# Kernel tuning notes

Measured on AMD Instinct MI355X. Metric: run time of the kernel, lower is better.

Reference implementation:

```python
import jax, jax.numpy as jnp
import numpy as np

N_G, N_U, E, C = 100000, 100000, 3200000, 2000000


def graph_conv(x, edges, W_rel, W_root, b):
    # PyG GraphConv (aggr='add'): out_i = (sum_{j->i} x_j) @ W_rel + x_i @ W_root + b
    src, dst = edges[0], edges[1]
    agg = jax.ops.segment_sum(x[src], dst, num_segments=x.shape[0])
    return agg @ W_rel + x @ W_root + b


def setup_inputs() -> dict:
    key = jax.random.key(0)
    ks = jax.random.split(key, 16)
    d = {
        'x_u': jax.random.normal(ks[0], (N_U, 4), jnp.float32),
        'x_g': jax.random.normal(ks[1], (N_G, 4), jnp.float32),
        'candidates': jax.random.randint(ks[2], (C, 2), 0, N_G + N_U, jnp.int64),
        'edges': jax.random.randint(ks[3], (2, E), 0, N_G, jnp.int64),
        # GraphConv(4,8)
        'W1_rel': jax.random.normal(ks[4], (4, 8), jnp.float32) * 0.5,
        'W1_root': jax.random.normal(ks[5], (4, 8), jnp.float32) * 0.5,
        'b1': jax.random.normal(ks[6], (8,), jnp.float32) * 0.1,
        # GraphConv(8,16)
        'W2_rel': jax.random.normal(ks[7], (8, 16), jnp.float32) * 0.35,
        'W2_root': jax.random.normal(ks[8], (8, 16), jnp.float32) * 0.35,
        'b2': jax.random.normal(ks[9], (16,), jnp.float32) * 0.1,
        # fc_unconnected: Linear(4,16) (Dropout is identity in eval)
        'W_un': jax.random.normal(ks[10], (4, 16), jnp.float32) * 0.5,
        'b_un': jax.random.normal(ks[11], (16,), jnp.float32) * 0.1,
        # fc: Linear(32,64) -> SELU -> Linear(64,1)
        'W_fc1': jax.random.normal(ks[12], (32, 64), jnp.float32) * 0.18,
        'b_fc1': jax.random.normal(ks[13], (64,), jnp.float32) * 0.1,
        'W_fc2': jax.random.normal(ks[14], (64, 1), jnp.float32) * 0.12,
        'b_fc2': jax.random.normal(ks[15], (1,), jnp.float32) * 0.1,
    }
    return d


def reference(x_u, x_g, candidates, edges,
              W1_rel, W1_root, b1, W2_rel, W2_root, b2,
              W_un, b_un, W_fc1, b_fc1, W_fc2, b_fc2):
    x_unconnected = x_u @ W_un + b_un                      # [N_u, 16]
    h = jax.nn.selu(graph_conv(x_g, edges, W1_rel, W1_root, b1))   # [N_g, 8]
    x_graph = jax.nn.selu(graph_conv(h, edges, W2_rel, W2_root, b2))  # [N_g, 16]
    x_stacked = jnp.concatenate([x_graph, x_unconnected], axis=0)  # [N_g+N_u, 16]
    ec = jnp.concatenate([x_stacked[candidates[:, 0]],
                          x_stacked[candidates[:, 1]]], axis=1)    # [C, 32]
    hidden = jax.nn.selu(ec @ W_fc1 + b_fc1)               # [C, 64]
    out = (hidden @ W_fc2 + b_fc2).squeeze(-1)             # [C]
    return out


if __name__ == '__main__':
    print(reference(**setup_inputs()).shape)
```

## Files before the change

### kernel.cpp

```cpp
#include <hip/hip_runtime.h>
#include <hip/hip_bf16.h>

#define NG 100000
#define NU 100000
#define NE 3200000
#define NC 2000000

#define BSZ 128
#define NBK 782
#define CAP 5120

#define NSUP 61
#define SFB 13
#define SSPAN (SFB * BSZ)
#define SCAP 56320
#define B1CH 4096
#define B2CH 4096

typedef __attribute__((ext_vector_type(8))) short short8;
typedef __attribute__((ext_vector_type(4))) float floatx4;
typedef unsigned short ushortx8 __attribute__((ext_vector_type(8)));

__device__ __forceinline__ float selu_f(float x) {
    const float LAM = 1.0507009873554805f;
    const float ALA = 1.7580993408473766f;
    const float L2E = 1.44269504088896340736f;
    float e = __builtin_amdgcn_exp2f(fminf(x, 0.f) * L2E);
    return fmaf(LAM, fmaxf(x, 0.f), fmaf(ALA, e, -ALA));
}

__device__ __forceinline__ float bfbits2f(unsigned short u) {
    return __uint_as_float(((unsigned)u) << 16);
}

__device__ __forceinline__ unsigned short f2bfbits(float f) {
    union { __hip_bfloat16 h; unsigned short u; } cv;
    cv.h = __float2bfloat16(f);
    return cv.u;
}

__device__ __forceinline__ float ldf(const void* p, int i, int isbf) {
    return isbf ? bfbits2f(((const unsigned short*)p)[i]) : ((const float*)p)[i];
}

__global__ void k_detect(const unsigned int* __restrict__ xw,
                         const unsigned int* __restrict__ cw,
                         const unsigned int* __restrict__ ew,
                         int* __restrict__ flags) {
    if (threadIdx.x != 0 || blockIdx.x != 0) return;
    int nb = 0;
    for (int i = 0; i < 64; ++i) {
        unsigned lo = xw[i] & 0xffffu;
        unsigned e = (lo >> 7) & 0xff;
        if (e >= 112 && e <= 134) ++nb;
    }
    flags[0] = (nb >= 32) ? 1 : 0;
    int cz = 0, ez = 0;
    for (int i = 0; i < 64; ++i) {
        if (cw[2 * i + 1] == 0u) ++cz;
        if (ew[2 * i + 1] == 0u) ++ez;
    }
    flags[1] = (cz >= 48) ? 1 : 0;
    flags[2] = (ez >= 48) ? 1 : 0;
}

__device__ __forceinline__ void ld_edge(const void* edges, long long e, int e64,
                                        int& s, int& d) {
    if (e64) {
        const long long* el = (const long long*)edges;
        s = (int)el[e];
        d = (int)el[NE + e];
    } else {
        const int* ei = (const int*)edges;
        s = ei[e];
        d = ei[NE + e];
    }
}

__global__ __launch_bounds__(256) void k_bin1(const void* __restrict__ edges,
        int* __restrict__ scur, unsigned int* __restrict__ slist,
        const int* __restrict__ flags) {
    __shared__ unsigned int tmp[B1CH];
    __shared__ unsigned char tsup[B1CH];
    __shared__ unsigned int ord[B1CH];
    __shared__ unsigned char osup[B1CH];
    __shared__ int hist[64];
    __shared__ int lstart[64];
    __shared__ int ofs[64];
    __shared__ int gbase[64];

    int tid = threadIdx.x;
    long long base = (long long)blockIdx.x * B1CH;
    int chunk = (int)(NE - base);
    if (chunk > B1CH) chunk = B1CH;
    int e64 = flags[2];

    if (tid < 64) hist[tid] = 0;
    __syncthreads();

    for (int i = 0; i < B1CH / 256; ++i) {
        int idx = i * 256 + tid;
        if (idx < chunk) {
            int s, d;
            ld_edge(edges, base + idx, e64, s, d);
            int sup = d / SSPAN;
            tmp[idx] = ((unsigned)s << 11) | (unsigned)(d - sup * SSPAN);
            tsup[idx] = (unsigned char)sup;
            atomicAdd(&hist[sup], 1);
        }
    }
    __syncthreads();

    if (tid == 0) {
        int run = 0;
        for (int b = 0; b < NSUP; ++b) {
            lstart[b] = run;
            run += hist[b];
        }
    }
    __syncthreads();
    if (tid < NSUP) {
        int c = hist[tid];
        int g = 0;
        if (c > 0) g = atomicAdd(&scur[tid], c);
        gbase[tid] = g;
        ofs[tid] = lstart[tid];
    }
    __syncthreads();

    for (int i = 0; i < B1CH / 256; ++i) {
        int idx = i * 256 + tid;
        if (idx < chunk) {
            int sup = tsup[idx];
            int pos = atomicAdd(&ofs[sup], 1);
            ord[pos] = tmp[idx];
            osup[pos] = (unsigned char)sup;
        }
    }
    __syncthreads();

    for (int i = 0; i < B1CH / 256; ++i) {
        int idx = i * 256 + tid;
        if (idx < chunk) {
            int sup = osup[idx];
            int p = gbase[sup] + (idx - lstart[sup]);
            if (p < SCAP) slist[(long long)sup * SCAP + p] = ord[idx];
        }
    }
}

#define SCH2 ((SCAP + B2CH - 1) / B2CH)

__global__ __launch_bounds__(256) void k_bin2(const int* __restrict__ scur,
        const unsigned int* __restrict__ slist,
        int* __restrict__ gcur, unsigned int* __restrict__ glist) {
    __shared__ unsigned int tmp[B2CH];
    __shared__ unsigned int ord[B2CH];
    __shared__ unsigned char ofid[B2CH];
    __shared__ int hist[16];
    __shared__ int lstart[16];
    __shared__ int ofs[16];
    __shared__ int gbase[16];

    int tid = threadIdx.x;
    int sup = blockIdx.x / SCH2;
    int ch = blockIdx.x % SCH2;
    int scnt = scur[sup];
    if (scnt > SCAP) scnt = SCAP;
    int start = ch * B2CH;
    int cnt = scnt - start;
    if (cnt <= 0) return;
    if (cnt > B2CH) cnt = B2CH;
    const unsigned int* sp = slist + (long long)sup * SCAP + start;

    if (tid < 16) hist[tid] = 0;
    __syncthreads();

    for (int i = 0; i < B2CH / 256; ++i) {
        int idx = i * 256 + tid;
        if (idx < cnt) {
            unsigned u = sp[idx];
            tmp[idx] = u;
            atomicAdd(&hist[(u & 2047) >> 7], 1);
        }
    }
    __syncthreads();

    if (tid == 0) {
        int run = 0;
        for (int b = 0; b < SFB; ++b) {
            lstart[b] = run;
            run += hist[b];
        }
    }
    __syncthreads();
    if (tid < SFB) {
        int c = hist[tid];
        int g = 0;
        int bf = sup * SFB + tid;
        if (c > 0 && bf < NBK) g = atomicAdd(&gcur[bf], c);
        gbase[tid] = g;
        ofs[tid] = lstart[tid];
    }
    __syncthreads();

    for (int i = 0; i < B2CH / 256; ++i) {
        int idx = i * 256 + tid;
        if (idx < cnt) {
            unsigned u = tmp[idx];
            int dl = u & 2047;
            int f = dl >> 7;
            int pos = atomicAdd(&ofs[f], 1);
            ord[pos] = ((u >> 11) << 7) | (unsigned)(dl & 127);
            ofid[pos] = (unsigned char)f;
        }
    }
    __syncthreads();

    for (int i = 0; i < B2CH / 256; ++i) {
        int idx = i * 256 + tid;
        if (idx < cnt) {
            int f = ofid[idx];
            int bf = sup * SFB + f;
            int p = gbase[f] + (idx - lstart[f]);
            if (p < CAP) glist[(long long)bf * CAP + p] = ord[idx];
        }
    }
}

__global__ __launch_bounds__(256) void k_sort(const int* __restrict__ gcur,
        unsigned int* __restrict__ glist,
        int* __restrict__ dstoff, int* __restrict__ ddeg) {
    __shared__ unsigned int tmp[CAP];
    __shared__ unsigned int sorted[CAP];
    __shared__ int hist[BSZ];
    __shared__ int incl[BSZ];
    __shared__ int cur[BSZ];
    int b = blockIdx.x;
    int tid = threadIdx.x;
    int cnt = gcur[b];
    if (cnt > CAP) cnt = CAP;
    unsigned int* lp = glist + (long long)b * CAP;

    if (tid < BSZ) hist[tid] = 0;
    __syncthreads();
    for (int k = tid; k < cnt; k += 256) {
        unsigned u = lp[k];
        tmp[k] = u;
        atomicAdd(&hist[u & 127], 1);
    }
    __syncthreads();
    if (tid < BSZ) incl[tid] = hist[tid];
    __syncthreads();
    for (int off = 1; off < BSZ; off <<= 1) {
        int v = (tid < BSZ && tid >= off) ? incl[tid - off] : 0;
        __syncthreads();
        if (tid < BSZ && tid >= off) incl[tid] += v;
        __syncthreads();
    }
    if (tid < BSZ) {
        int excl = incl[tid] - hist[tid];
        cur[tid] = excl;
        int d = b * BSZ + tid;
        if (d < NG) {
            dstoff[d] = b * CAP + excl;
            ddeg[d] = hist[tid];
        }
    }
    __syncthreads();
    for (int k = tid; k < cnt; k += 256) {
        unsigned u = tmp[k];
        int pos = atomicAdd(&cur[u & 127], 1);
        sorted[pos] = u >> 7;
    }
    __syncthreads();
    for (int k = tid; k < cnt; k += 256) lp[k] = sorted[k];
}

__global__ __launch_bounds__(256) void k_gather1(const int* __restrict__ dstoff,
        const int* __restrict__ ddeg, const unsigned int* __restrict__ glist,
        const void* __restrict__ xg,
        const void* __restrict__ W1r, const void* __restrict__ W1o,
        const void* __restrict__ b1, unsigned short* __restrict__ hbf,
        const int* __restrict__ flags) {
    int gid = blockIdx.x * 256 + threadIdx.x;
    int d = gid >> 4;
    if (d >= NG) return;
    int q = gid & 15;
    int isbf = flags[0];
    int start = dstoff[d];
    int deg = ddeg[d];
    float a0 = 0.f, a1 = 0.f, a2 = 0.f, a3 = 0.f;
    if (isbf) {
        const unsigned short* xp = (const unsigned short*)xg;
        int k = q;
        for (; k + 16 < deg; k += 32) {
            int s0 = glist[start + k];
            int s1 = glist[start + k + 16];
            ushort4 r0 = *(const ushort4*)(xp + s0 * 4);
            ushort4 r1 = *(const ushort4*)(xp + s1 * 4);
            a0 += bfbits2f(r0.x) + bfbits2f(r1.x);
            a1 += bfbits2f(r0.y) + bfbits2f(r1.y);
            a2 += bfbits2f(r0.z) + bfbits2f(r1.z);
            a3 += bfbits2f(r0.w) + bfbits2f(r1.w);
        }
        for (; k < deg; k += 16) {
            int s = glist[start + k];
            ushort4 r = *(const ushort4*)(xp + s * 4);
            a0 += bfbits2f(r.x); a1 += bfbits2f(r.y);
            a2 += bfbits2f(r.z); a3 += bfbits2f(r.w);
        }
    } else {
        const float* xp = (const float*)xg;
        int k = q;
        for (; k + 16 < deg; k += 32) {
            int s0 = glist[start + k];
            int s1 = glist[start + k + 16];
            float4 r0 = *(const float4*)(xp + s0 * 4);
            float4 r1 = *(const float4*)(xp + s1 * 4);
            a0 += r0.x + r1.x;
            a1 += r0.y + r1.y;
            a2 += r0.z + r1.z;
            a3 += r0.w + r1.w;
        }
        for (; k < deg; k += 16) {
            int s = glist[start + k];
            float4 r = *(const float4*)(xp + s * 4);
            a0 += r.x; a1 += r.y; a2 += r.z; a3 += r.w;
        }
    }
#pragma unroll
    for (int off = 1; off < 16; off <<= 1) {
        a0 += __shfl_xor(a0, off);
        a1 += __shfl_xor(a1, off);
        a2 += __shfl_xor(a2, off);
        a3 += __shfl_xor(a3, off);
    }
    if (q < 8) {
        float a[4] = {a0, a1, a2, a3};
        float v = ldf(b1, q, isbf);
#pragma unroll
        for (int c = 0; c < 4; ++c)
            v += a[c] * ldf(W1r, c * 8 + q, isbf)
               + ldf(xg, d * 4 + c, isbf) * ldf(W1o, c * 8 + q, isbf);
        hbf[d * 8 + q] = f2bfbits(selu_f(v));
    }
}

__global__ __launch_bounds__(256) void k_gather2(const int* __restrict__ dstoff,
        const int* __restrict__ ddeg, const unsigned int* __restrict__ glist,
        const ushortx8* __restrict__ hbf,
        const void* __restrict__ W2r, const void* __restrict__ W2o,
        const void* __restrict__ b2, unsigned short* __restrict__ xs,
        const int* __restrict__ flags) {
    int gid = blockIdx.x * 256 + threadIdx.x;
    int d = gid >> 4;
    if (d >= NG) return;
    int q = gid & 15;
    int isbf = flags[0];
    int start = dstoff[d];
    int deg = ddeg[d];
    float a[8] = {0.f, 0.f, 0.f, 0.f, 0.f, 0.f, 0.f, 0.f};
    int k = q;
    for (; k + 16 < deg; k += 32) {
        int s0 = glist[start + k];
        int s1 = glist[start + k + 16];
        ushortx8 r0 = hbf[s0];
        ushortx8 r1 = hbf[s1];
#pragma unroll
        for (int c = 0; c < 8; ++c)
            a[c] += bfbits2f((unsigned short)r0[c]) + bfbits2f((unsigned short)r1[c]);
    }
    for (; k < deg; k += 16) {
        int s = glist[start + k];
        ushortx8 r = hbf[s];
#pragma unroll
        for (int c = 0; c < 8; ++c) a[c] += bfbits2f((unsigned short)r[c]);
    }
#pragma unroll
    for (int off = 1; off < 16; off <<= 1) {
#pragma unroll
        for (int c = 0; c < 8; ++c) a[c] += __shfl_xor(a[c], off);
    }
    ushortx8 hr = hbf[d];
    float hv[8];
#pragma unroll
    for (int c = 0; c < 8; ++c) hv[c] = bfbits2f((unsigned short)hr[c]);
    float v = ldf(b2, q, isbf);
#pragma unroll
    for (int c = 0; c < 8; ++c)
        v += a[c] * ldf(W2r, c * 16 + q, isbf)
           + hv[c] * ldf(W2o, c * 16 + q, isbf);
    xs[d * 16 + q] = f2bfbits(selu_f(v));
}

__global__ __launch_bounds__(256) void k_unconn(const void* __restrict__ xu,
        const void* __restrict__ Wun, const void* __restrict__ bun,
        unsigned short* __restrict__ xs, const int* __restrict__ flags) {
    int u = blockIdx.x * 256 + threadIdx.x;
    if (u >= NU) return;
    int isbf = flags[0];
    float x[4];
#pragma unroll
    for (int k = 0; k < 4; ++k) x[k] = ldf(xu, u * 4 + k, isbf);
    ushortx8 lo, hi;
#pragma unroll
    for (int j = 0; j < 16; ++j) {
        float v = ldf(bun, j, isbf);
#pragma unroll
        for (int k = 0; k < 4; ++k)
            v += x[k] * ldf(Wun, k * 16 + j, isbf);
        unsigned short bb = f2bfbits(v);
        if (j < 8) lo[j] = bb; else hi[j - 8] = bb;
    }
    ushortx8* xp = (ushortx8*)(xs + (NG + u) * 16);
    xp[0] = lo;
    xp[1] = hi;
}

__device__ __forceinline__ int ld_candrow(const void* cand, int c, int hp, int c64) {
    const int* ci = (const int*)cand;
    return c64 ? ci[(2 * c + hp) * 2] : ci[2 * c + hp];
}

__global__ __launch_bounds__(256, 5) void k_fc(const unsigned short* __restrict__ xs,
        const void* __restrict__ cand,
        const void* __restrict__ Wfc1, const void* __restrict__ bfc1,
        const void* __restrict__ Wfc2, const void* __restrict__ bfc2,
        void* __restrict__ out, const int* __restrict__ flags) {
    const float LAM = 1.0507009873554805f;
    const float ALA = 1.7580993408473766f;
    const float L2E = 1.44269504088896340736f;
    const float AR2 = 1.6732632423543772f * 1.44269504088896340736f;
    const float SCL = 1.0507009873554805f / 1.44269504088896340736f;
    int lane = threadIdx.x & 63;
    int wid = (blockIdx.x * blockDim.x + threadIdx.x) >> 6;
    int m = lane & 15;
    int half = lane >> 4;
    int isbf = flags[0], c64 = flags[1];

    short8 wfrag[4];
    floatx4 cbias[4];
    float w2s[4][4];
    float c_corr;
    if (isbf) {
        const unsigned short* W1p = (const unsigned short*)Wfc1;
#pragma unroll
        for (int t = 0; t < 4; ++t)
#pragma unroll
            for (int j = 0; j < 8; ++j)
                wfrag[t][j] = (short)f2bfbits(
                    bfbits2f(W1p[(half * 8 + j) * 64 + t * 16 + m]) * L2E);
        const unsigned short* b1p = (const unsigned short*)bfc1;
        const unsigned short* w2p = (const unsigned short*)Wfc2;
        float asum = 0.f;
#pragma unroll
        for (int t = 0; t < 4; ++t)
#pragma unroll
            for (int r = 0; r < 4; ++r) {
                int h = t * 16 + half * 4 + r;
                cbias[t][r] = bfbits2f(b1p[h]) * L2E;
                float w2 = bfbits2f(w2p[h]);
                w2s[t][r] = w2 * SCL;
                asum += w2 * ALA;
            }
        asum += __shfl_xor(asum, 16, 64);
        asum += __shfl_xor(asum, 32, 64);
        c_corr = bfbits2f(((const unsigned short*)bfc2)[0]) - asum;
    } else {
        const float* W1p = (const float*)Wfc1;
#pragma unroll
        for (int t = 0; t < 4; ++t)
#pragma unroll
            for (int j = 0; j < 8; ++j)
                wfrag[t][j] = (short)f2bfbits(
                    W1p[(half * 8 + j) * 64 + t * 16 + m] * L2E);
        const float* b1p = (const float*)bfc1;
        const float* w2p = (const float*)Wfc2;
        float asum = 0.f;
#pragma unroll
        for (int t = 0; t < 4; ++t)
#pragma unroll
            for (int r = 0; r < 4; ++r) {
                int h = t * 16 + half * 4 + r;
                cbias[t][r] = b1p[h] * L2E;
                float w2 = w2p[h];
                w2s[t][r] = w2 * SCL;
                asum += w2 * ALA;
            }
        asum += __shfl_xor(asum, 16, 64);
        asum += __shfl_xor(asum, 32, 64);
        c_corr = ((const float*)bfc2)[0] - asum;
    }

    const int nTiles = NC / 16;
    int nW = (gridDim.x * blockDim.x) >> 6;
    if (wid >= nTiles) return;

    int half1 = half & 1;
    int hp = half >> 1;
    int t1 = wid + nW, t2 = wid + 2 * nW, t3 = wid + 3 * nW, t4 = wid + 4 * nW;
    int r0i = ld_candrow(cand, wid * 16 + m, hp, c64);
    int r1i = ld_candrow(cand, ((t1 < nTiles) ? t1 : wid) * 16 + m, hp, c64);
    int r2i = ld_candrow(cand, ((t2 < nTiles) ? t2 : wid) * 16 + m, hp, c64);
    int r3i = ld_candrow(cand, ((t3 < nTiles) ? t3 : wid) * 16 + m, hp, c64);
    int r4i = ld_candrow(cand, ((t4 < nTiles) ? t4 : wid) * 16 + m, hp, c64);
    {
        short8 af0 = *(const short8*)(xs + r0i * 16 + half1 * 8);
        short8 af1 = *(const short8*)(xs + r1i * 16 + half1 * 8);
        short8 af2 = *(const short8*)(xs + r2i * 16 + half1 * 8);
        short8 af3 = *(const short8*)(xs + r3i * 16 + half1 * 8);

#pragma unroll 2
        for (int t = wid; t < nTiles; t += nW) {
            int tn5 = t + 5 * nW;
            int r5i = ld_candrow(cand, ((tn5 < nTiles) ? tn5 : t) * 16 + m, hp, c64);
            short8 af4 = *(const short8*)(xs + r4i * 16 + half1 * 8);

            float ps[4];
#pragma unroll
            for (int tt = 0; tt < 4; ++tt) {
                floatx4 ac = __builtin_amdgcn_mfma_f32_16x16x32_bf16(
                    wfrag[tt], af0, cbias[tt], 0, 0, 0);
                float s = 0.f;
#pragma unroll
                for (int r = 0; r < 4; ++r) {
                    float v = ac[r];
                    float mx = fmaxf(v, 0.f);
                    float e = __builtin_amdgcn_exp2f(fminf(v, 0.f));
                    s = fmaf(w2s[tt][r], fmaf(AR2, e, mx), s);
                }
                ps[tt] = s;
            }
            float part = (ps[0] + ps[1]) + (ps[2] + ps[3]);
            part += __shfl_xor(part, 16, 64);
            part += __shfl_xor(part, 32, 64);
            if (half == 0) {
                float o = part + c_corr;
                if (isbf) ((unsigned short*)out)[t * 16 + m] = f2bfbits(o);
                else ((float*)out)[t * 16 + m] = o;
            }
            af0 = af1;
            af1 = af2;
            af2 = af3;
            af3 = af4;
            r4i = r5i;
        }
    }
}

extern "C" void kernel_launch(void* const* d_in, const int* in_sizes, int n_in,
                              void* d_out, int out_size, void* d_ws, size_t ws_size,
                              hipStream_t stream) {
    const void* x_u = d_in[0];
    const void* x_g = d_in[1];
    const void* cand = d_in[2];
    const void* edges = d_in[3];
    const void* W1r = d_in[4];
    const void* W1o = d_in[5];
    const void* b1 = d_in[6];
    const void* W2r = d_in[7];
    const void* W2o = d_in[8];
    const void* b2 = d_in[9];
    const void* Wun = d_in[10];
    const void* bun = d_in[11];
    const void* Wfc1 = d_in[12];
    const void* bfc1 = d_in[13];
    const void* Wfc2 = d_in[14];
    const void* bfc2 = d_in[15];

    char* ws = (char*)d_ws;
    int* flags = (int*)ws;
    int* gcur = (int*)(ws + 64);
    int* scur = (int*)(ws + 3264);
    unsigned int* glist = (unsigned int*)(ws + 4160);
    size_t glist_bytes = (size_t)NBK * CAP * 4;
    char* p = ws + 4160 + glist_bytes;
    unsigned int* slist = (unsigned int*)p;
    int* dstoff = (int*)p;
    int* ddeg = (int*)(p + 400000);
    unsigned short* hbf = (unsigned short*)(p + 800000);
    unsigned short* xs = (unsigned short*)(p + 2400000);

    hipMemsetAsync(gcur, 0, 3456, stream);

    k_detect<<<1, 64, 0, stream>>>((const unsigned int*)x_u,
                                   (const unsigned int*)cand,
                                   (const unsigned int*)edges, flags);
    k_bin1<<<(NE + B1CH - 1) / B1CH, 256, 0, stream>>>(edges, scur, slist, flags);
    k_bin2<<<NSUP * SCH2, 256, 0, stream>>>(scur, slist, gcur, glist);
    k_sort<<<NBK, 256, 0, stream>>>(gcur, glist, dstoff, ddeg);
    k_gather1<<<(16 * NG + 255) / 256, 256, 0, stream>>>(dstoff, ddeg, glist, x_g,
                                                         W1r, W1o, b1, hbf, flags);
    k_gather2<<<(16 * NG + 255) / 256, 256, 0, stream>>>(dstoff, ddeg, glist,
                                                         (const ushortx8*)hbf,
                                                         W2r, W2o, b2, xs, flags);
    k_unconn<<<(NU + 255) / 256, 256, 0, stream>>>(x_u, Wun, bun, xs, flags);
    k_fc<<<1280, 256, 0, stream>>>(xs, cand, Wfc1, bfc1, Wfc2, bfc2, d_out, flags);
}
```

Measured before the change: 268.7 us.

## Collapse two-pass edge binning into single pass directly into dst buckets

```diff
diff --git a/kernel.cpp b/kernel.cpp
--- a/kernel.cpp
+++ b/kernel.cpp
@@ -9,13 +9,7 @@
 #define BSZ 128
 #define NBK 782
 #define CAP 5120
-
-#define NSUP 61
-#define SFB 13
-#define SSPAN (SFB * BSZ)
-#define SCAP 56320
 #define B1CH 4096
-#define B2CH 4096
 
 typedef __attribute__((ext_vector_type(8))) short short8;
 typedef __attribute__((ext_vector_type(4))) float floatx4;
@@ -47,21 +41,17 @@
                          const unsigned int* __restrict__ cw,
                          const unsigned int* __restrict__ ew,
                          int* __restrict__ flags) {
-    if (threadIdx.x != 0 || blockIdx.x != 0) return;
-    int nb = 0;
-    for (int i = 0; i < 64; ++i) {
-        unsigned lo = xw[i] & 0xffffu;
-        unsigned e = (lo >> 7) & 0xff;
-        if (e >= 112 && e <= 134) ++nb;
-    }
-    flags[0] = (nb >= 32) ? 1 : 0;
-    int cz = 0, ez = 0;
-    for (int i = 0; i < 64; ++i) {
-        if (cw[2 * i + 1] == 0u) ++cz;
-        if (ew[2 * i + 1] == 0u) ++ez;
-    }
-    flags[1] = (cz >= 48) ? 1 : 0;
-    flags[2] = (ez >= 48) ? 1 : 0;
+    int lane = threadIdx.x;
+    unsigned lo = xw[lane] & 0xffffu;
+    unsigned e = (lo >> 7) & 0xff;
+    unsigned long long m1 = __ballot(e >= 112 && e <= 134);
+    unsigned long long m2 = __ballot(cw[2 * lane + 1] == 0u);
+    unsigned long long m3 = __ballot(ew[2 * lane + 1] == 0u);
+    if (lane == 0) {
+        flags[0] = (__popcll(m1) >= 32) ? 1 : 0;
+        flags[1] = (__popcll(m2) >= 48) ? 1 : 0;
+        flags[2] = (__popcll(m3) >= 48) ? 1 : 0;
+    }
 }
 
 __device__ __forceinline__ void ld_edge(const void* edges, long long e, int e64,
@@ -78,16 +68,13 @@
 }
 
 __global__ __launch_bounds__(256) void k_bin1(const void* __restrict__ edges,
-        int* __restrict__ scur, unsigned int* __restrict__ slist,
+        int* __restrict__ gcur, unsigned int* __restrict__ glist,
         const int* __restrict__ flags) {
     __shared__ unsigned int tmp[B1CH];
-    __shared__ unsigned char tsup[B1CH];
-    __shared__ unsigned int ord[B1CH];
-    __shared__ unsigned char osup[B1CH];
-    __shared__ int hist[64];
-    __shared__ int lstart[64];
-    __shared__ int ofs[64];
-    __shared__ int gbase[64];
+    __shared__ unsigned short tfid[B1CH];
+    __shared__ int hist[NBK];
+    __shared__ int gbase[NBK];
+    __shared__ int ofs[NBK];
 
     int tid = threadIdx.x;
     long long base = (long long)blockIdx.x * B1CH;
@@ -95,7 +82,7 @@
     if (chunk > B1CH) chunk = B1CH;
     int e64 = flags[2];
 
-    if (tid < 64) hist[tid] = 0;
+    for (int b = tid; b < NBK; b += 256) hist[b] = 0;
     __syncthreads();
 
     for (int i = 0; i < B1CH / 256; ++i) {
@@ -103,127 +90,28 @@
         if (idx < chunk) {
             int s, d;
             ld_edge(edges, base + idx, e64, s, d);
-            int sup = d / SSPAN;
-            tmp[idx] = ((unsigned)s << 11) | (unsigned)(d - sup * SSPAN);
-            tsup[idx] = (unsigned char)sup;
-            atomicAdd(&hist[sup], 1);
-        }
-    }
-    __syncthreads();
-
-    if (tid == 0) {
-        int run = 0;
-        for (int b = 0; b < NSUP; ++b) {
-            lstart[b] = run;
-            run += hist[b];
-        }
-    }
-    __syncthreads();
-    if (tid < NSUP) {
-        int c = hist[tid];
-        int g = 0;
-        if (c > 0) g = atomicAdd(&scur[tid], c);
-        gbase[tid] = g;
-        ofs[tid] = lstart[tid];
+            int f = d >> 7;
+            tmp[idx] = ((unsigned)s << 7) | (unsigned)(d & 127);
+            tfid[idx] = (unsigned short)f;
+            atomicAdd(&hist[f], 1);
+        }
+    }
+    __syncthreads();
+
+    for (int b = tid; b < NBK; b += 256) {
+        int c = hist[b];
+        gbase[b] = (c > 0) ? atomicAdd(&gcur[b], c) : 0;
+        ofs[b] = 0;
     }
     __syncthreads();
 
     for (int i = 0; i < B1CH / 256; ++i) {
         int idx = i * 256 + tid;
         if (idx < chunk) {
-            int sup = tsup[idx];
-            int pos = atomicAdd(&ofs[sup], 1);
-            ord[pos] = tmp[idx];
-            osup[pos] = (unsigned char)sup;
-        }
-    }
-    __syncthreads();
-
-    for (int i = 0; i < B1CH / 256; ++i) {
-        int idx = i * 256 + tid;
-        if (idx < chunk) {
-            int sup = osup[idx];
-            int p = gbase[sup] + (idx - lstart[sup]);
-            if (p < SCAP) slist[(long long)sup * SCAP + p] = ord[idx];
-        }
-    }
-}
-
-#define SCH2 ((SCAP + B2CH - 1) / B2CH)
-
-__global__ __launch_bounds__(256) void k_bin2(const int* __restrict__ scur,
-        const unsigned int* __restrict__ slist,
-        int* __restrict__ gcur, unsigned int* __restrict__ glist) {
-    __shared__ unsigned int tmp[B2CH];
-    __shared__ unsigned int ord[B2CH];
-    __shared__ unsigned char ofid[B2CH];
-    __shared__ int hist[16];
-    __shared__ int lstart[16];
-    __shared__ int ofs[16];
-    __shared__ int gbase[16];
-
-    int tid = threadIdx.x;
-    int sup = blockIdx.x / SCH2;
-    int ch = blockIdx.x % SCH2;
-    int scnt = scur[sup];
-    if (scnt > SCAP) scnt = SCAP;
-    int start = ch * B2CH;
-    int cnt = scnt - start;
-    if (cnt <= 0) return;
-    if (cnt > B2CH) cnt = B2CH;
-    const unsigned int* sp = slist + (long long)sup * SCAP + start;
-
-    if (tid < 16) hist[tid] = 0;
-    __syncthreads();
-
-    for (int i = 0; i < B2CH / 256; ++i) {
-        int idx = i * 256 + tid;
-        if (idx < cnt) {
-            unsigned u = sp[idx];
-            tmp[idx] = u;
-            atomicAdd(&hist[(u & 2047) >> 7], 1);
-        }
-    }
-    __syncthreads();
-
-    if (tid == 0) {
-        int run = 0;
-        for (int b = 0; b < SFB; ++b) {
-            lstart[b] = run;
-            run += hist[b];
-        }
-    }
-    __syncthreads();
-    if (tid < SFB) {
-        int c = hist[tid];
-        int g = 0;
-        int bf = sup * SFB + tid;
-        if (c > 0 && bf < NBK) g = atomicAdd(&gcur[bf], c);
-        gbase[tid] = g;
-        ofs[tid] = lstart[tid];
-    }
-    __syncthreads();
-
-    for (int i = 0; i < B2CH / 256; ++i) {
-        int idx = i * 256 + tid;
-        if (idx < cnt) {
-            unsigned u = tmp[idx];
-            int dl = u & 2047;
-            int f = dl >> 7;
+            int f = tfid[idx];
             int pos = atomicAdd(&ofs[f], 1);
-            ord[pos] = ((u >> 11) << 7) | (unsigned)(dl & 127);
-            ofid[pos] = (unsigned char)f;
-        }
-    }
-    __syncthreads();
-
-    for (int i = 0; i < B2CH / 256; ++i) {
-        int idx = i * 256 + tid;
-        if (idx < cnt) {
-            int f = ofid[idx];
-            int bf = sup * SFB + f;
-            int p = gbase[f] + (idx - lstart[f]);
-            if (p < CAP) glist[(long long)bf * CAP + p] = ord[idx];
+            int p = gbase[f] + pos;
+            if (p < CAP) glist[(long long)f * CAP + p] = tmp[idx];
         }
     }
 }
@@ -234,8 +122,8 @@
     __shared__ unsigned int tmp[CAP];
     __shared__ unsigned int sorted[CAP];
     __shared__ int hist[BSZ];
-    __shared__ int incl[BSZ];
     __shared__ int cur[BSZ];
+    __shared__ int wtot;
     int b = blockIdx.x;
     int tid = threadIdx.x;
     int cnt = gcur[b];
@@ -250,21 +138,23 @@
         atomicAdd(&hist[u & 127], 1);
     }
     __syncthreads();
-    if (tid < BSZ) incl[tid] = hist[tid];
-    __syncthreads();
-    for (int off = 1; off < BSZ; off <<= 1) {
-        int v = (tid < BSZ && tid >= off) ? incl[tid - off] : 0;
-        __syncthreads();
-        if (tid < BSZ && tid >= off) incl[tid] += v;
-        __syncthreads();
-    }
+    int h = (tid < BSZ) ? hist[tid] : 0;
+    int s = h;
+#pragma unroll
+    for (int off = 1; off < 64; off <<= 1) {
+        int v = __shfl_up(s, off, 64);
+        if ((tid & 63) >= off) s += v;
+    }
+    if (tid == 63) wtot = s;
+    __syncthreads();
+    if (tid >= 64 && tid < BSZ) s += wtot;
     if (tid < BSZ) {
-        int excl = incl[tid] - hist[tid];
+        int excl = s - h;
         cur[tid] = excl;
         int d = b * BSZ + tid;
         if (d < NG) {
             dstoff[d] = b * CAP + excl;
-            ddeg[d] = hist[tid];
+            ddeg[d] = h;
         }
     }
     __syncthreads();
@@ -572,23 +462,20 @@
     char* ws = (char*)d_ws;
     int* flags = (int*)ws;
     int* gcur = (int*)(ws + 64);
-    int* scur = (int*)(ws + 3264);
     unsigned int* glist = (unsigned int*)(ws + 4160);
     size_t glist_bytes = (size_t)NBK * CAP * 4;
     char* p = ws + 4160 + glist_bytes;
-    unsigned int* slist = (unsigned int*)p;
     int* dstoff = (int*)p;
     int* ddeg = (int*)(p + 400000);
     unsigned short* hbf = (unsigned short*)(p + 800000);
     unsigned short* xs = (unsigned short*)(p + 2400000);
 
-    hipMemsetAsync(gcur, 0, 3456, stream);
+    hipMemsetAsync(gcur, 0, 3200, stream);
 
     k_detect<<<1, 64, 0, stream>>>((const unsigned int*)x_u,
                                    (const unsigned int*)cand,
                                    (const unsigned int*)edges, flags);
-    k_bin1<<<(NE + B1CH - 1) / B1CH, 256, 0, stream>>>(edges, scur, slist, flags);
-    k_bin2<<<NSUP * SCH2, 256, 0, stream>>>(scur, slist, gcur, glist);
+    k_bin1<<<(NE + B1CH - 1) / B1CH, 256, 0, stream>>>(edges, gcur, glist, flags);
     k_sort<<<NBK, 256, 0, stream>>>(gcur, glist, dstoff, ddeg);
     k_gather1<<<(16 * NG + 255) / 256, 256, 0, stream>>>(dstoff, ddeg, glist, x_g,
                                                          W1r, W1o, b1, hbf, flags);
```

Result: faster. 256.7 us (-4.5%).
